# Optimization experiments

Measured on AMD Instinct MI355X. Metric: run time of the kernel, lower is better.

## Reference

```python
import jax, jax.numpy as jnp
import numpy as np

DIM = 1024
HEADS = 16
DIM_HEAD = 64
INNER = HEADS * DIM_HEAD  # 1024
SCALE = DIM_HEAD ** -0.5


def layernorm(x, gamma, beta, eps=1e-5):
    mu = jnp.mean(x, axis=-1, keepdims=True)
    var = jnp.var(x, axis=-1, keepdims=True)
    return (x - mu) * jax.lax.rsqrt(var + eps) * gamma + beta


def setup_inputs() -> dict:
    key = jax.random.key(0)
    ks = jax.random.split(key, 6)
    x = jax.random.normal(ks[0], (2, 2048, DIM), dtype=jnp.float32)
    # params (stored [in, out]; torch Linear does x @ W.T with W [out, in])
    w_q = jax.random.normal(ks[1], (DIM, INNER), dtype=jnp.float32) * (DIM ** -0.5)
    w_kv = jax.random.normal(ks[2], (DIM, 2 * INNER), dtype=jnp.float32) * (DIM ** -0.5)
    w_out = jax.random.normal(ks[3], (INNER, DIM), dtype=jnp.float32) * (INNER ** -0.5)
    b_out = jnp.zeros((DIM,), dtype=jnp.float32)
    gamma = jnp.ones((DIM,), dtype=jnp.float32)
    beta = jnp.zeros((DIM,), dtype=jnp.float32)
    return {"x": x, "w_q": w_q, "w_kv": w_kv, "w_out": w_out, "b_out": b_out,
            "gamma": gamma, "beta": beta}


def reference(x, w_q, w_kv, w_out, b_out, gamma, beta):
    b, n, _ = x.shape
    xn = layernorm(x, gamma, beta)
    q = xn @ w_q                           # [b, n, inner]
    kv = xn @ w_kv                         # [b, n, 2*inner]
    k, v = jnp.split(kv, 2, axis=-1)
    def split_heads(t):
        return t.reshape(b, n, HEADS, DIM_HEAD).transpose(0, 2, 1, 3)  # b h n d
    q, k, v = split_heads(q), split_heads(k), split_heads(v)
    dots = jnp.einsum('bhid,bhjd->bhij', q, k) * SCALE   # [b, h, n, n]
    attn = jax.nn.softmax(dots, axis=-1)
    out = jnp.einsum('bhij,bhjd->bhid', attn, v)          # [b, h, n, d]
    out = out.transpose(0, 2, 1, 3).reshape(b, n, INNER)  # b n (h d)
    return out @ w_out + b_out
```

## Files before the change

### kernel.cpp

```cpp
#include <hip/hip_runtime.h>

typedef unsigned short u16;
typedef u16   u16x8 __attribute__((ext_vector_type(8)));
typedef __bf16 bf16x8 __attribute__((ext_vector_type(8)));
typedef float f32x4 __attribute__((ext_vector_type(4)));
typedef _Float16 f16x4 __attribute__((ext_vector_type(4)));
typedef unsigned u32x2 __attribute__((ext_vector_type(2)));

__device__ __forceinline__ u16 f2b(float f){ __bf16 h=(__bf16)f; return __builtin_bit_cast(u16,h); }

__device__ __forceinline__ f32x4 mfma16(u16x8 a, u16x8 b, f32x4 c){
  return __builtin_amdgcn_mfma_f32_16x16x32_bf16(
      __builtin_bit_cast(bf16x8,a), __builtin_bit_cast(bf16x8,b), c, 0,0,0);
}

__device__ __forceinline__ void gl2lds16(const u16* g, u16* l){
  __builtin_amdgcn_global_load_lds((const __attribute__((address_space(1))) void*)g,
                                   (__attribute__((address_space(3))) void*)l, 16, 0, 0);
}

__global__ __launch_bounds__(256) void ln_kernel(const float* __restrict__ x,
                                                 const float* __restrict__ gamma,
                                                 const float* __restrict__ beta,
                                                 u16* __restrict__ xn){
  const int row = blockIdx.x, t = threadIdx.x;
  const float4 v = ((const float4*)(x + (size_t)row*1024))[t];
  float s  = v.x+v.y+v.z+v.w;
  float sq = v.x*v.x+v.y*v.y+v.z*v.z+v.w*v.w;
  for (int m=1;m<64;m<<=1){ s += __shfl_xor(s,m); sq += __shfl_xor(sq,m); }
  __shared__ float red[8];
  const int w=t>>6, l=t&63;
  if(l==0){ red[w]=s; red[4+w]=sq; }
  __syncthreads();
  const float S  = red[0]+red[1]+red[2]+red[3];
  const float SQ = red[4]+red[5]+red[6]+red[7];
  const float mu = S*(1.f/1024.f);
  const float var= SQ*(1.f/1024.f)-mu*mu;
  const float rs = rsqrtf(var+1e-5f);
  const float4 g4=((const float4*)gamma)[t], b4=((const float4*)beta)[t];
  u16 o0=f2b((v.x-mu)*rs*g4.x+b4.x);
  u16 o1=f2b((v.y-mu)*rs*g4.y+b4.y);
  u16 o2=f2b((v.z-mu)*rs*g4.z+b4.z);
  u16 o3=f2b((v.w-mu)*rs*g4.w+b4.w);
  uint2 p; p.x=(unsigned)o0|((unsigned)o1<<16); p.y=(unsigned)o2|((unsigned)o3<<16);
  ((uint2*)(xn + (size_t)row*1024))[t]=p;
}

__global__ __launch_bounds__(256) void wtrans_all_kernel(const float* __restrict__ wq,
    const float* __restrict__ wkv, const float* __restrict__ wout,
    u16* __restrict__ wqkvt, u16* __restrict__ woutt){
  __shared__ float tile[64][65];
  const int bx=blockIdx.x, t=threadIdx.x;
  const float* in; u16* out; int C, cxx;
  if(bx<16){ in=wq;  out=wqkvt;           C=1024; cxx=bx; }
  else if(bx<48){ in=wkv; out=wqkvt+1024*1024; C=2048; cxx=bx-16; }
  else { in=wout; out=woutt;             C=1024; cxx=bx-48; }
  const int R=1024;
  const int c0=cxx*64, r0=blockIdx.y*64;
  {
    const int r=t>>2, cc=t&3;
    const float* gp = in + (size_t)(r0+r)*C + c0 + cc*16;
    #pragma unroll
    for(int i=0;i<4;i++){
      float4 f=((const float4*)gp)[i];
      tile[r][cc*16+i*4+0]=f.x; tile[r][cc*16+i*4+1]=f.y;
      tile[r][cc*16+i*4+2]=f.z; tile[r][cc*16+i*4+3]=f.w;
    }
  }
  __syncthreads();
  const int c=t>>2, rc=t&3;
  u16x8 a,b;
  #pragma unroll
  for(int i=0;i<8;i++) a[i]=f2b(tile[rc*16+i][c]);
  #pragma unroll
  for(int i=0;i<8;i++) b[i]=f2b(tile[rc*16+8+i][c]);
  u16* op = out + (size_t)(c0+c)*R + r0 + rc*16;
  *(u16x8*)op=a; *(u16x8*)(op+8)=b;
}

__global__ __launch_bounds__(256) void vpack_kernel(const u16* __restrict__ kv,
                                                    u16* __restrict__ vp){
  __shared__ u16 tile[64][72];
  const int tok0=blockIdx.x*64, h=blockIdx.y, bb=blockIdx.z, t=threadIdx.x;
  {
    const int r=t>>2, cc=t&3;
    const u16* gp = kv + (size_t)(bb*2048 + tok0 + r)*2048 + 1024 + h*64 + cc*16;
    *(u16x8*)&tile[r][cc*16]   = *(const u16x8*)gp;
    *(u16x8*)&tile[r][cc*16+8] = *(const u16x8*)(gp+8);
  }
  __syncthreads();
  const int d=t&63, j4s=t>>6;
  #pragma unroll
  for(int pass=0;pass<4;pass++){
    const int j4=pass*4+j4s;
    u16 pk[4];
    #pragma unroll
    for(int jj=0;jj<4;jj++){
      const unsigned bits=((unsigned)tile[j4*4+jj][d])<<16;
      const _Float16 hh=(_Float16)__builtin_bit_cast(float,bits);
      pk[jj]=__builtin_bit_cast(u16,hh);
    }
    uint2 w2; w2.x=(unsigned)pk[0]|((unsigned)pk[1]<<16); w2.y=(unsigned)pk[2]|((unsigned)pk[3]<<16);
    *(uint2*)&vp[((size_t)(bb*16+h)*512 + (tok0>>2) + j4)*256 + d*4]=w2;
  }
}

template<int MODE,int TM>
__global__ __launch_bounds__(256) void gemm_bt_kernel(const u16* __restrict__ A,
    const u16* __restrict__ Bt, u16* __restrict__ outQ, u16* __restrict__ outKV,
    float* __restrict__ outF, const float* __restrict__ bias, float scale,
    int M, int N, int K){
  constexpr int MT = TM/32;
  __shared__ u16 As[TM*64];
  __shared__ u16 Bs[128*64];
  const int t=threadIdx.x, w=t>>6, l=t&63, qd=l>>4, ln=l&15;
  const int m0=blockIdx.y*TM, n0=blockIdx.x*128;
  const int wm=(w>>1)*(TM/2), wn=(w&1)*64;
  f32x4 acc[MT][4] = {};
  const int nK = K>>6;
  for(int kt=0; kt<nK; kt++){
    const int k0=kt*64;
    #pragma unroll
    for(int p=0;p<MT;p++){
      const int cid=p*256+t, r=cid>>3, pc=cid&7, g=pc^(r&7);
      gl2lds16(A + (size_t)(m0+r)*K + k0 + g*8, &As[(p*256 + (t&192))*8]);
    }
    #pragma unroll
    for(int p=0;p<4;p++){
      const int cid=p*256+t, r=cid>>3, pc=cid&7, g=pc^(r&7);
      gl2lds16(Bt + (size_t)(n0+r)*K + k0 + g*8, &Bs[(p*256 + (t&192))*8]);
    }
    __syncthreads();
    #pragma unroll
    for(int ks=0;ks<2;ks++){
      u16x8 af[MT], bf[4];
      #pragma unroll
      for(int mt=0;mt<MT;mt++){
        const int m=wm+mt*16+ln, kc=ks*4+qd, pcc=kc^(m&7);
        af[mt]=*(const u16x8*)&As[m*64 + pcc*8];
      }
      #pragma unroll
      for(int nt=0;nt<4;nt++){
        const int n=wn+nt*16+ln, kc=ks*4+qd, pcc=kc^(n&7);
        bf[nt]=*(const u16x8*)&Bs[n*64 + pcc*8];
      }
      #pragma unroll
      for(int mt=0;mt<MT;mt++)
        #pragma unroll
        for(int nt=0;nt<4;nt++)
          acc[mt][nt]=mfma16(af[mt],bf[nt],acc[mt][nt]);
    }
    __syncthreads();
  }
  #pragma unroll
  for(int mt=0;mt<MT;mt++)
    #pragma unroll
    for(int rr=0;rr<4;rr++){
      const int row = m0+wm+mt*16+qd*4+rr;
      #pragma unroll
      for(int nt=0;nt<4;nt++){
        const int col = n0+wn+nt*16+ln;
        const float v = acc[mt][nt][rr];
        if(MODE==1){
          outF[(size_t)row*N+col]=v+bias[col];
        }else{
          if(col<1024) outQ[(size_t)row*1024+col]=f2b(v*scale);
          else         outKV[(size_t)row*2048+(col-1024)]=f2b(v);
        }
      }
    }
}

__global__ __launch_bounds__(256,3) void attn_kernel(const u16* __restrict__ Q,
    const u16* __restrict__ Kb, const u16* __restrict__ Vp, u16* __restrict__ O){
  __shared__ u16 Ks[8192];
  __shared__ u16 Vs[8192];
  const int qt=blockIdx.x, h=blockIdx.y, bb=blockIdx.z;
  const int t=threadIdx.x, w=t>>6, l=t&63, qd=l>>4, ln=l&15;
  const int q0=qt*128;
  const size_t baseQ=(size_t)bb*2048*1024 + h*64;
  const size_t baseK=(size_t)bb*2048*2048 + h*64;
  const size_t baseV=(size_t)(bb*16+h)*131072;
  u16x8 qf[2][2];
  #pragma unroll
  for(int it=0;it<2;it++)
    #pragma unroll
    for(int ks=0;ks<2;ks++)
      qf[it][ks] = *(const u16x8*)(Q + baseQ + (size_t)(q0+w*32+it*16+ln)*1024 + ks*32+qd*8);
  float l_i[2]={0.f,0.f};
  f32x4 o_acc[2][4]={};

  for(int j0=0;j0<2048;j0+=128){
    __syncthreads();
    #pragma unroll
    for(int p=0;p<4;p++){
      const int r=(p*256+t)>>3, g=(t&7)^((t>>3)&7);
      gl2lds16(Kb + baseK + (size_t)(j0+r)*2048 + g*8, &Ks[(p*256+(t&192))*8]);
    }
    #pragma unroll
    for(int p=0;p<4;p++){
      gl2lds16(Vp + baseV + (size_t)(j0>>2)*256 + (size_t)(p*256+t)*8,
               &Vs[(p*256+(t&192))*8]);
    }
    __syncthreads();

    #pragma unroll
    for(int jh=0;jh<2;jh++){
      f32x4 s[2][4]={};
      #pragma unroll
      for(int ks=0;ks<2;ks++){
        u16x8 kf[4];
        #pragma unroll
        for(int j4=0;j4<4;j4++){
          const int row=(jh*4+j4)*16+ln;
          kf[j4]=*(const u16x8*)&Ks[row*64 + (((ks*4+qd)^(ln&7))*8)];
        }
        #pragma unroll
        for(int j4=0;j4<4;j4++){
          s[0][j4]=mfma16(kf[j4],qf[0][ks],s[0][j4]);
          s[1][j4]=mfma16(kf[j4],qf[1][ks],s[1][j4]);
        }
      }
      #pragma unroll
      for(int j4=0;j4<4;j4++){
        const int vrow=((jh*4+j4)*4+qd)*256;
        f16x4 vf[4];
        #pragma unroll
        for(int dt=0;dt<4;dt++) vf[dt]=*(const f16x4*)&Vs[vrow + (dt*16+ln)*4];
        #pragma unroll
        for(int it=0;it<2;it++){
          float p0=exp2f(s[it][j4][0]), p1=exp2f(s[it][j4][1]);
          float p2=exp2f(s[it][j4][2]), p3=exp2f(s[it][j4][3]);
          l_i[it]+= (p0+p1)+(p2+p3);
          const auto lo=__builtin_amdgcn_cvt_pkrtz(p0,p1);
          const auto hi=__builtin_amdgcn_cvt_pkrtz(p2,p3);
          u32x2 pu; pu.x=__builtin_bit_cast(unsigned,lo); pu.y=__builtin_bit_cast(unsigned,hi);
          const f16x4 pf=__builtin_bit_cast(f16x4,pu);
          #pragma unroll
          for(int dt=0;dt<4;dt++)
            o_acc[it][dt]=__builtin_amdgcn_mfma_f32_16x16x16f16(pf,vf[dt],o_acc[it][dt],0,0,0);
        }
      }
    }
  }

  #pragma unroll
  for(int it=0;it<2;it++){
    l_i[it]+=__shfl_xor(l_i[it],16);
    l_i[it]+=__shfl_xor(l_i[it],32);
    const float linv=1.f/l_i[it];
    #pragma unroll
    for(int rr=0;rr<4;rr++){
      const float lr=__shfl(linv,qd*4+rr);
      const int row=q0+w*32+it*16+qd*4+rr;
      #pragma unroll
      for(int dt=0;dt<4;dt++)
        O[baseQ + (size_t)row*1024 + dt*16+ln]=f2b(o_acc[it][dt][rr]*lr);
    }
  }
}

extern "C" void kernel_launch(void* const* d_in, const int* in_sizes, int n_in,
                              void* d_out, int out_size, void* d_ws, size_t ws_size,
                              hipStream_t stream) {
  const float* x     = (const float*)d_in[0];
  const float* w_q   = (const float*)d_in[1];
  const float* w_kv  = (const float*)d_in[2];
  const float* w_out = (const float*)d_in[3];
  const float* b_out = (const float*)d_in[4];
  const float* gamma = (const float*)d_in[5];
  const float* beta  = (const float*)d_in[6];
  float* out = (float*)d_out;

  char* ws=(char*)d_ws;
  size_t off=0;
  u16* xn    =(u16*)(ws+off); off += (size_t)4096*1024*2;
  u16* wqkvt =(u16*)(ws+off); off += (size_t)3072*1024*2;
  u16* woutt =(u16*)(ws+off); off += (size_t)1024*1024*2;
  u16* qb    =(u16*)(ws+off); off += (size_t)4096*1024*2;
  u16* kvb   =(u16*)(ws+off); off += (size_t)4096*2048*2;
  u16* vpb   =(u16*)(ws+off); off += (size_t)4096*1024*2;
  u16* ob    =(u16*)(ws+off); off += (size_t)4096*1024*2;

  ln_kernel<<<4096,256,0,stream>>>(x,gamma,beta,xn);
  wtrans_all_kernel<<<dim3(64,16),256,0,stream>>>(w_q,w_kv,w_out,wqkvt,woutt);

  const float SCALE_Q = 0.125f*1.4426950408889634f;
  gemm_bt_kernel<2,128><<<dim3(24,32),256,0,stream>>>(xn,wqkvt,qb,kvb,nullptr,nullptr,SCALE_Q,4096,3072,1024);
  vpack_kernel<<<dim3(32,16,2),256,0,stream>>>(kvb,vpb);
  attn_kernel<<<dim3(16,16,2),256,0,stream>>>(qb,kvb,vpb,ob);
  gemm_bt_kernel<1,64><<<dim3(8,64),256,0,stream>>>(ob,woutt,nullptr,nullptr,out,b_out,1.f,4096,1024,1024);
}
```

Baseline: 212.1 us.

## Repack V for 16-byte LDS reads and simplify GEMM epilogue branching

```diff
diff --git a/kernel.cpp b/kernel.cpp
--- a/kernel.cpp
+++ b/kernel.cpp
@@ -4,7 +4,9 @@
 typedef u16   u16x8 __attribute__((ext_vector_type(8)));
 typedef __bf16 bf16x8 __attribute__((ext_vector_type(8)));
 typedef float f32x4 __attribute__((ext_vector_type(4)));
+typedef float f32x2 __attribute__((ext_vector_type(2)));
 typedef _Float16 f16x4 __attribute__((ext_vector_type(4)));
+typedef _Float16 f16x8 __attribute__((ext_vector_type(8)));
 typedef unsigned u32x2 __attribute__((ext_vector_type(2)));
 
 __device__ __forceinline__ u16 f2b(float f){ __bf16 h=(__bf16)f; return __builtin_bit_cast(u16,h); }
@@ -89,19 +91,24 @@
     *(u16x8*)&tile[r][cc*16+8] = *(const u16x8*)(gp+8);
   }
   __syncthreads();
-  const int d=t&63, j4s=t>>6;
-  #pragma unroll
-  for(int pass=0;pass<4;pass++){
-    const int j4=pass*4+j4s;
-    u16 pk[4];
-    #pragma unroll
-    for(int jj=0;jj<4;jj++){
-      const unsigned bits=((unsigned)tile[j4*4+jj][d])<<16;
-      const _Float16 hh=(_Float16)__builtin_bit_cast(float,bits);
-      pk[jj]=__builtin_bit_cast(u16,hh);
-    }
-    uint2 w2; w2.x=(unsigned)pk[0]|((unsigned)pk[1]<<16); w2.y=(unsigned)pk[2]|((unsigned)pk[3]<<16);
-    *(uint2*)&vp[((size_t)(bb*16+h)*512 + (tok0>>2) + j4)*256 + d*4]=w2;
+  const int d=t&63, sl=t>>6;
+  #pragma unroll
+  for(int pass=0;pass<2;pass++){
+    const int combo=pass*4+sl;
+    const int j32l=combo>>2, qd=combo&3;
+    u16 pk[8];
+    #pragma unroll
+    for(int tt=0;tt<2;tt++)
+      #pragma unroll
+      for(int rr=0;rr<4;rr++){
+        const unsigned bits=((unsigned)tile[j32l*32+tt*16+qd*4+rr][d])<<16;
+        const _Float16 hh=(_Float16)__builtin_bit_cast(float,bits);
+        pk[tt*4+rr]=__builtin_bit_cast(u16,hh);
+      }
+    uint4 w4;
+    w4.x=(unsigned)pk[0]|((unsigned)pk[1]<<16); w4.y=(unsigned)pk[2]|((unsigned)pk[3]<<16);
+    w4.z=(unsigned)pk[4]|((unsigned)pk[5]<<16); w4.w=(unsigned)pk[6]|((unsigned)pk[7]<<16);
+    *(uint4*)&vp[((((size_t)(bb*16+h))*64 + (tok0>>5) + j32l)*4 + qd)*512 + d*8]=w4;
   }
 }
 
@@ -152,23 +159,32 @@
     }
     __syncthreads();
   }
-  #pragma unroll
-  for(int mt=0;mt<MT;mt++)
-    #pragma unroll
-    for(int rr=0;rr<4;rr++){
-      const int row = m0+wm+mt*16+qd*4+rr;
-      #pragma unroll
-      for(int nt=0;nt<4;nt++){
-        const int col = n0+wn+nt*16+ln;
-        const float v = acc[mt][nt][rr];
-        if(MODE==1){
-          outF[(size_t)row*N+col]=v+bias[col];
-        }else{
-          if(col<1024) outQ[(size_t)row*1024+col]=f2b(v*scale);
-          else         outKV[(size_t)row*2048+(col-1024)]=f2b(v);
+  if(MODE==1){
+    #pragma unroll
+    for(int mt=0;mt<MT;mt++)
+      #pragma unroll
+      for(int rr=0;rr<4;rr++){
+        const int row = m0+wm+mt*16+qd*4+rr;
+        #pragma unroll
+        for(int nt=0;nt<4;nt++){
+          const int col = n0+wn+nt*16+ln;
+          outF[(size_t)row*N+col]=acc[mt][nt][rr]+bias[col];
         }
       }
-    }
+  } else {
+    u16* outp; int ostr; float sc;
+    if(n0<1024){ outp=outQ+n0; ostr=1024; sc=scale; }
+    else       { outp=outKV+(n0-1024); ostr=2048; sc=1.f; }
+    #pragma unroll
+    for(int mt=0;mt<MT;mt++)
+      #pragma unroll
+      for(int rr=0;rr<4;rr++){
+        const int row = m0+wm+mt*16+qd*4+rr;
+        #pragma unroll
+        for(int nt=0;nt<4;nt++)
+          outp[(size_t)row*ostr + wn+nt*16+ln]=f2b(acc[mt][nt][rr]*sc);
+      }
+  }
 }
 
 __global__ __launch_bounds__(256,3) void attn_kernel(const u16* __restrict__ Q,
@@ -187,8 +203,9 @@
     #pragma unroll
     for(int ks=0;ks<2;ks++)
       qf[it][ks] = *(const u16x8*)(Q + baseQ + (size_t)(q0+w*32+it*16+ln)*1024 + ks*32+qd*8);
-  float l_i[2]={0.f,0.f};
+  f32x2 l2[2]={{0.f,0.f},{0.f,0.f}};
   f32x4 o_acc[2][4]={};
+  const f32x4 zf={0.f,0.f,0.f,0.f};
 
   for(int j0=0;j0<2048;j0+=128){
     __syncthreads();
@@ -199,14 +216,14 @@
     }
     #pragma unroll
     for(int p=0;p<4;p++){
-      gl2lds16(Vp + baseV + (size_t)(j0>>2)*256 + (size_t)(p*256+t)*8,
+      gl2lds16(Vp + baseV + (size_t)(j0>>5)*2048 + (size_t)(p*256+t)*8,
                &Vs[(p*256+(t&192))*8]);
     }
     __syncthreads();
 
     #pragma unroll
     for(int jh=0;jh<2;jh++){
-      f32x4 s[2][4]={};
+      f32x4 s[2][4];
       #pragma unroll
       for(int ks=0;ks<2;ks++){
         u16x8 kf[4];
@@ -217,28 +234,45 @@
         }
         #pragma unroll
         for(int j4=0;j4<4;j4++){
-          s[0][j4]=mfma16(kf[j4],qf[0][ks],s[0][j4]);
-          s[1][j4]=mfma16(kf[j4],qf[1][ks],s[1][j4]);
+          if(ks==0){
+            s[0][j4]=mfma16(kf[j4],qf[0][0],zf);
+            s[1][j4]=mfma16(kf[j4],qf[1][0],zf);
+          }else{
+            s[0][j4]=mfma16(kf[j4],qf[0][1],s[0][j4]);
+            s[1][j4]=mfma16(kf[j4],qf[1][1],s[1][j4]);
+          }
         }
       }
       #pragma unroll
-      for(int j4=0;j4<4;j4++){
-        const int vrow=((jh*4+j4)*4+qd)*256;
-        f16x4 vf[4];
-        #pragma unroll
-        for(int dt=0;dt<4;dt++) vf[dt]=*(const f16x4*)&Vs[vrow + (dt*16+ln)*4];
-        #pragma unroll
-        for(int it=0;it<2;it++){
-          float p0=exp2f(s[it][j4][0]), p1=exp2f(s[it][j4][1]);
-          float p2=exp2f(s[it][j4][2]), p3=exp2f(s[it][j4][3]);
-          l_i[it]+= (p0+p1)+(p2+p3);
-          const auto lo=__builtin_amdgcn_cvt_pkrtz(p0,p1);
-          const auto hi=__builtin_amdgcn_cvt_pkrtz(p2,p3);
-          u32x2 pu; pu.x=__builtin_bit_cast(unsigned,lo); pu.y=__builtin_bit_cast(unsigned,hi);
-          const f16x4 pf=__builtin_bit_cast(f16x4,pu);
+      for(int al=0;al<2;al++){
+        const int a=jh*2+al;
+        f16x8 vf2[4];
+        #pragma unroll
+        for(int dt=0;dt<4;dt++)
+          vf2[dt]=*(const f16x8*)&Vs[((a*4+qd)*64 + dt*16+ln)*8];
+        #pragma unroll
+        for(int tt=0;tt<2;tt++){
+          const int j4l=al*2+tt;
+          f16x4 vf[4];
           #pragma unroll
           for(int dt=0;dt<4;dt++)
-            o_acc[it][dt]=__builtin_amdgcn_mfma_f32_16x16x16f16(pf,vf[dt],o_acc[it][dt],0,0,0);
+            vf[dt]=tt? __builtin_shufflevector(vf2[dt],vf2[dt],4,5,6,7)
+                     : __builtin_shufflevector(vf2[dt],vf2[dt],0,1,2,3);
+          #pragma unroll
+          for(int it=0;it<2;it++){
+            const float p0=exp2f(s[it][j4l][0]), p1=exp2f(s[it][j4l][1]);
+            const float p2=exp2f(s[it][j4l][2]), p3=exp2f(s[it][j4l][3]);
+            f32x2 pa; pa.x=p0; pa.y=p1;
+            f32x2 pb; pb.x=p2; pb.y=p3;
+            l2[it]+=pa+pb;
+            const auto lo=__builtin_amdgcn_cvt_pkrtz(p0,p1);
+            const auto hi=__builtin_amdgcn_cvt_pkrtz(p2,p3);
+            u32x2 pu; pu.x=__builtin_bit_cast(unsigned,lo); pu.y=__builtin_bit_cast(unsigned,hi);
+            const f16x4 pf=__builtin_bit_cast(f16x4,pu);
+            #pragma unroll
+            for(int dt=0;dt<4;dt++)
+              o_acc[it][dt]=__builtin_amdgcn_mfma_f32_16x16x16f16(pf,vf[dt],o_acc[it][dt],0,0,0);
+          }
         }
       }
     }
@@ -246,9 +280,10 @@
 
   #pragma unroll
   for(int it=0;it<2;it++){
-    l_i[it]+=__shfl_xor(l_i[it],16);
-    l_i[it]+=__shfl_xor(l_i[it],32);
-    const float linv=1.f/l_i[it];
+    float li=l2[it].x+l2[it].y;
+    li+=__shfl_xor(li,16);
+    li+=__shfl_xor(li,32);
+    const float linv=1.f/li;
     #pragma unroll
     for(int rr=0;rr<4;rr++){
       const float lr=__shfl(linv,qd*4+rr);
```

After: 209.6 us. No clear change (-1.2%).
